# Kernel optimization log

Hardware: AMD Instinct MI355X
Metric: run time of the kernel (lower is better)

The kernel has to match this reference:

```python
import jax, jax.numpy as jnp
import numpy as np
import math

B, S, D, H, HD, FF, L, NS = 16, 512, 256, 8, 32, 1024, 2, 1024
THETA = 10000.0
EPS = 1e-5


def setup_inputs() -> dict:
    key = jax.random.key(0)
    ks = jax.random.split(key, 20)
    n = lambda i, shape: jax.random.normal(ks[i], shape, jnp.float32) * 0.02
    inp = {
        'values': jax.random.normal(ks[0], (B, S), jnp.float32),
        'dib': jax.random.uniform(ks[1], (B, S), jnp.float32),
        'gamma': jax.random.uniform(ks[2], (B, S), jnp.float32),
        'memory_type': jnp.ones((B, S), jnp.float32),
        'key_padding_mask': jnp.ones((B, S), dtype=bool),
        # input projection Linear(5, D)
        'in_w': n(3, (5, D)), 'in_b': jnp.zeros((D,), jnp.float32),
        # per-layer params stacked on leading L axis
        'ln1_s': jnp.ones((L, D), jnp.float32), 'ln1_b': jnp.zeros((L, D), jnp.float32),
        'qw': n(4, (L, D, D)), 'qb': jnp.zeros((L, D), jnp.float32),
        'kw': n(5, (L, D, D)), 'kb': jnp.zeros((L, D), jnp.float32),
        'vw': n(6, (L, D, D)), 'vb': jnp.zeros((L, D), jnp.float32),
        'ow': n(7, (L, D, D)), 'ob': jnp.zeros((L, D), jnp.float32),
        'ln2_s': jnp.ones((L, D), jnp.float32), 'ln2_b': jnp.zeros((L, D), jnp.float32),
        'ffw1': n(8, (L, D, FF)), 'ffb1': jnp.zeros((L, FF), jnp.float32),
        'ffw2': n(9, (L, FF, D)), 'ffb2': jnp.zeros((L, D), jnp.float32),
        'fn_s': jnp.ones((D,), jnp.float32), 'fn_b': jnp.zeros((D,), jnp.float32),
        # output head Linear(S*D, NS)
        'head_w': n(10, (S * D, NS)), 'head_b': jnp.zeros((NS,), jnp.float32),
    }
    return inp


def _layernorm(x, s, b):
    m = jnp.mean(x, axis=-1, keepdims=True)
    v = jnp.mean(jnp.square(x - m), axis=-1, keepdims=True)
    return (x - m) * jax.lax.rsqrt(v + EPS) * s + b


def _rotate_half(x):
    x1, x2 = jnp.split(x, 2, axis=-1)
    return jnp.concatenate((-x2, x1), axis=-1)


def _rope_tables():
    pos = jnp.arange(S, dtype=jnp.float32)
    inv_freq = 1.0 / (THETA ** (jnp.arange(0, HD, 2, dtype=jnp.float32) / HD))
    freqs = pos[:, None] * inv_freq[None, :]           # [S, HD/2]
    emb = jnp.concatenate((freqs, freqs), axis=-1)      # [S, HD]
    return jnp.cos(emb), jnp.sin(emb)


def _forward(values, dib, gamma, memory_type, key_padding_mask,
             in_w, in_b, ln1_s, ln1_b, qw, qb, kw, kb, vw, vb, ow, ob,
             ln2_s, ln2_b, ffw1, ffb1, ffw2, ffb2, fn_s, fn_b, head_w, head_b):
    # token features: (sign, magnitude, gamma, dib, memory_type in {-1,+1})
    sign = jnp.where(values >= 0, 1.0, -1.0)
    mt = memory_type * 2.0 - 1.0  # values in [0,1] -> signed encoding
    features = jnp.stack((sign, jnp.abs(values), gamma, dib, mt), axis=-1)  # [B,S,5]
    x = features @ in_w + in_b  # [B,S,D]

    cos, sin = _rope_tables()  # [S,HD]
    cos4 = cos[None, None]     # [1,1,S,HD]
    sin4 = sin[None, None]
    mask = key_padding_mask    # [B,S] bool
    neg = jnp.finfo(x.dtype).min
    scale = 1.0 / math.sqrt(HD)

    for l in range(L):
        h = _layernorm(x, ln1_s[l], ln1_b[l])
        q = (h @ qw[l] + qb[l]).reshape(B, S, H, HD).transpose(0, 2, 1, 3)  # [B,H,S,HD]
        k = (h @ kw[l] + kb[l]).reshape(B, S, H, HD).transpose(0, 2, 1, 3)
        v = (h @ vw[l] + vb[l]).reshape(B, S, H, HD).transpose(0, 2, 1, 3)
        q = q * cos4 + _rotate_half(q) * sin4
        k = k * cos4 + _rotate_half(k) * sin4
        scores = jnp.einsum('bhqd,bhkd->bhqk', q, k) * scale  # [B,H,S,S]
        scores = jnp.where(mask[:, None, None, :], scores, neg)
        attn = jax.nn.softmax(scores, axis=-1)
        ctx = jnp.einsum('bhqk,bhkd->bhqd', attn, v)
        ctx = ctx.transpose(0, 2, 1, 3).reshape(B, S, D)
        out = (ctx @ ow[l] + ob[l]) * mask[..., None].astype(x.dtype)
        x = x + out
        h2 = _layernorm(x, ln2_s[l], ln2_b[l])
        ff = jax.nn.gelu(h2 @ ffw1[l] + ffb1[l], approximate=False) @ ffw2[l] + ffb2[l]
        x = x + ff

    x = _layernorm(x, fn_s, fn_b)
    logits = x.reshape(B, S * D) @ head_w + head_b  # [B,NS]
    return logits


def reference(values, dib, gamma, memory_type, key_padding_mask,
              in_w, in_b, ln1_s, ln1_b, qw, qb, kw, kb, vw, vb, ow, ob,
              ln2_s, ln2_b, ffw1, ffb1, ffw2, ffb2, fn_s, fn_b, head_w, head_b):
    return _forward(values, dib, gamma, memory_type, key_padding_mask,
                    in_w, in_b, ln1_s, ln1_b, qw, qb, kw, kb, vw, vb, ow, ob,
                    ln2_s, ln2_b, ffw1, ffb1, ffw2, ffb2, fn_s, fn_b, head_w, head_b)
```

## Files before the change

kernel.cpp:

```cpp
#include <hip/hip_runtime.h>
#include <math.h>

#define BB 16
#define SS 512
#define DD 256
#define HH 8
#define HDIM 32
#define FFD 1024
#define NL 2
#define NSOUT 1024
#define SD (SS*DD)
#define ROWS (BB*SS)

#define HEAD_KC 256
#define HEAD_NCH 512

typedef __attribute__((ext_vector_type(8))) short short8;
typedef __attribute__((ext_vector_type(4))) float f32x4;

__device__ __forceinline__ unsigned short f2bf(float f) {
    union { float f; unsigned u; } c; c.f = f;
    unsigned u = c.u + 0x7fffu + ((c.u >> 16) & 1u);
    return (unsigned short)(u >> 16);
}

__global__ __launch_bounds__(256) void k_prep_all(
    const float* __restrict__ p_qw, const float* __restrict__ p_kw,
    const float* __restrict__ p_vw, const float* __restrict__ p_ow,
    const float* __restrict__ p_f1w, const float* __restrict__ p_f2w,
    unsigned short* __restrict__ wq, unsigned short* __restrict__ wk,
    unsigned short* __restrict__ wv, unsigned short* __restrict__ wo,
    unsigned short* __restrict__ wf1, unsigned short* __restrict__ wf2,
    float* __restrict__ ct, float* __restrict__ st) {
    int bid = blockIdx.x;
    int t = threadIdx.x;
    if (bid >= 1536) {
        int i = (bid - 1536) * 256 + t;
        if (i < SS * 16) {
            int s = i >> 4, f = i & 15;
            float invf = powf(10000.f, -(float)f / 16.f);
            float ang = (float)s * invf;
            ct[i] = cosf(ang);
            st[i] = sinf(ang);
        }
        return;
    }
    const float* src; unsigned short* dst;
    int K, N, kx, nx, l;
    if (bid < 512) {
        int grp = bid >> 7, r = bid & 127; l = r >> 6; int tl = r & 63;
        kx = tl >> 3; nx = tl & 7; K = DD; N = DD;
        src = grp == 0 ? p_qw : grp == 1 ? p_kw : grp == 2 ? p_vw : p_ow;
        dst = grp == 0 ? wq : grp == 1 ? wk : grp == 2 ? wv : wo;
    } else if (bid < 1024) {
        int r = bid - 512; l = r >> 8; int tl = r & 255;
        kx = tl >> 5; nx = tl & 31; K = DD; N = FFD; src = p_f1w; dst = wf1;
    } else {
        int r = bid - 1024; l = r >> 8; int tl = r & 255;
        kx = tl >> 3; nx = tl & 7; K = FFD; N = DD; src = p_f2w; dst = wf2;
    }
    __shared__ float tile[32][33];
    size_t zo = (size_t)l * K * N;
    int k0 = kx * 32, n0 = nx * 32;
    int r_ = t >> 3, c4 = (t & 7) * 4;
    float4 a = *(const float4*)&src[zo + (size_t)(k0 + r_) * N + n0 + c4];
    tile[r_][c4 + 0] = a.x; tile[r_][c4 + 1] = a.y; tile[r_][c4 + 2] = a.z; tile[r_][c4 + 3] = a.w;
    __syncthreads();
    unsigned o0 = f2bf(tile[c4 + 0][r_]), o1 = f2bf(tile[c4 + 1][r_]);
    unsigned o2 = f2bf(tile[c4 + 2][r_]), o3 = f2bf(tile[c4 + 3][r_]);
    uint2 ud = { o0 | (o1 << 16), o2 | (o3 << 16) };
    *(uint2*)&dst[zo + (size_t)(n0 + r_) * K + k0 + c4] = ud;
}

__global__ __launch_bounds__(256) void k_input_proj(
    const float* __restrict__ values, const float* __restrict__ dib,
    const float* __restrict__ gamma, const float* __restrict__ mtyp,
    const float* __restrict__ in_w, const float* __restrict__ in_b,
    float* __restrict__ x) {
    int i = blockIdx.x * 256 + threadIdx.x;
    int row = i >> 6, d4 = (i & 63) * 4;
    float v = values[row];
    float f0 = (v >= 0.f) ? 1.f : -1.f;
    float f1 = fabsf(v);
    float f2 = gamma[row];
    float f3 = dib[row];
    float f4 = mtyp[row] * 2.f - 1.f;
    float4 w0 = *(const float4*)&in_w[d4];
    float4 w1 = *(const float4*)&in_w[DD + d4];
    float4 w2 = *(const float4*)&in_w[2 * DD + d4];
    float4 w3 = *(const float4*)&in_w[3 * DD + d4];
    float4 w4 = *(const float4*)&in_w[4 * DD + d4];
    float4 bb = *(const float4*)&in_b[d4];
    float4 o;
    o.x = f0 * w0.x + f1 * w1.x + f2 * w2.x + f3 * w3.x + f4 * w4.x + bb.x;
    o.y = f0 * w0.y + f1 * w1.y + f2 * w2.y + f3 * w3.y + f4 * w4.y + bb.y;
    o.z = f0 * w0.z + f1 * w1.z + f2 * w2.z + f3 * w3.z + f4 * w4.z + bb.z;
    o.w = f0 * w0.w + f1 * w1.w + f2 * w2.w + f3 * w3.w + f4 * w4.w + bb.w;
    *(float4*)&x[(size_t)row * DD + d4] = o;
}

template <bool OBF>
__global__ __launch_bounds__(256) void k_layernorm_w(
    const float* __restrict__ in, void* __restrict__ outp,
    const float* __restrict__ sc, const float* __restrict__ bi) {
    int t = threadIdx.x, lane = t & 63, w = t >> 6;
    int row = blockIdx.x * 4 + w;
    float4 v = *(const float4*)&in[(size_t)row * DD + lane * 4];
    float s1 = v.x + v.y + v.z + v.w;
    float s2 = v.x * v.x + v.y * v.y + v.z * v.z + v.w * v.w;
#pragma unroll
    for (int off = 32; off > 0; off >>= 1) {
        s1 += __shfl_xor(s1, off);
        s2 += __shfl_xor(s2, off);
    }
    float mean = s1 * (1.f / DD);
    float var = s2 * (1.f / DD) - mean * mean;
    float rstd = rsqrtf(var + 1e-5f);
    float4 sv = *(const float4*)&sc[lane * 4];
    float4 bv = *(const float4*)&bi[lane * 4];
    float o0 = (v.x - mean) * rstd * sv.x + bv.x;
    float o1 = (v.y - mean) * rstd * sv.y + bv.y;
    float o2 = (v.z - mean) * rstd * sv.z + bv.z;
    float o3 = (v.w - mean) * rstd * sv.w + bv.w;
    if (OBF) {
        ushort4 u = { f2bf(o0), f2bf(o1), f2bf(o2), f2bf(o3) };
        *(ushort4*)&((unsigned short*)outp)[(size_t)row * DD + lane * 4] = u;
    } else {
        float4 o = { o0, o1, o2, o3 };
        *(float4*)&((float*)outp)[(size_t)row * DD + lane * 4] = o;
    }
}

__global__ __launch_bounds__(256) void k_gemm_ff1(
    const short* __restrict__ A, const short* __restrict__ Bt,
    const float* __restrict__ bias, unsigned short* __restrict__ Cout,
    int M, int N, int K) {
    __shared__ __align__(16) short As[128 * 32];
    __shared__ __align__(16) short Bs[128 * 32];
    int t = threadIdx.x;
    int lane = t & 63, wid = t >> 6;
    int wr = wid >> 1, wc = wid & 1;
    int m0 = blockIdx.x * 128, n0 = blockIdx.y * 128;
    f32x4 acc[4][4] = {};
    int srow = t >> 2, sslot = t & 3;
    for (int k0 = 0; k0 < K; k0 += 32) {
#pragma unroll
        for (int p = 0; p < 2; ++p) {
            int row = srow + p * 64;
            int sw = sslot ^ ((row >> 1) & 3);
            *(float4*)&As[row * 32 + sw * 8] =
                *(const float4*)&A[(size_t)(m0 + row) * K + k0 + sslot * 8];
            *(float4*)&Bs[row * 32 + sw * 8] =
                *(const float4*)&Bt[(size_t)(n0 + row) * K + k0 + sslot * 8];
        }
        __syncthreads();
        short8 af[4], bfr[4];
#pragma unroll
        for (int mt = 0; mt < 4; ++mt) {
            int row = wr * 64 + mt * 16 + (lane & 15);
            int sl = (lane >> 4) ^ ((row >> 1) & 3);
            af[mt] = *(const short8*)&As[row * 32 + sl * 8];
        }
#pragma unroll
        for (int nt = 0; nt < 4; ++nt) {
            int row = wc * 64 + nt * 16 + (lane & 15);
            int sl = (lane >> 4) ^ ((row >> 1) & 3);
            bfr[nt] = *(const short8*)&Bs[row * 32 + sl * 8];
        }
#pragma unroll
        for (int mt = 0; mt < 4; ++mt)
#pragma unroll
            for (int nt = 0; nt < 4; ++nt)
                acc[mt][nt] = __builtin_amdgcn_mfma_f32_16x16x32_bf16(af[mt], bfr[nt], acc[mt][nt], 0, 0, 0);
        __syncthreads();
    }
#pragma unroll
    for (int mt = 0; mt < 4; ++mt) {
#pragma unroll
        for (int i = 0; i < 4; ++i) {
            int gm = m0 + wr * 64 + mt * 16 + (lane >> 4) * 4 + i;
#pragma unroll
            for (int nt = 0; nt < 4; ++nt) {
                int gn = n0 + wc * 64 + nt * 16 + (lane & 15);
                float v = acc[mt][nt][i] + bias[gn];
                v = 0.5f * v * (1.f + erff(v * 0.70710678118654752f));
                Cout[(size_t)gm * N + gn] = f2bf(v);
            }
        }
    }
}

template <int EPI>
__global__ __launch_bounds__(256) void k_gemm64(
    const short* __restrict__ A, const short* __restrict__ Bt,
    const float* __restrict__ bias, float* __restrict__ Cout,
    int M, int N, int K, const float* __restrict__ resx, const int* __restrict__ mask) {
    __shared__ __align__(16) short As[64 * 64];
    __shared__ __align__(16) short Bs[128 * 64];
    int t = threadIdx.x;
    int lane = t & 63, wid = t >> 6;
    int wr = wid >> 1, wc = wid & 1;
    int m0 = blockIdx.x * 64, n0 = blockIdx.y * 128;
    int l15 = lane & 15, lh = lane >> 4;
    f32x4 acc[2][4] = {};
    for (int k0 = 0; k0 < K; k0 += 64) {
#pragma unroll
        for (int p = 0; p < 2; ++p) {
            int idx = t + p * 256;
            int row = idx >> 3, sl = idx & 7;
            int sw = sl ^ (row & 7);
            *(float4*)&As[row * 64 + sw * 8] =
                *(const float4*)&A[(size_t)(m0 + row) * K + k0 + sl * 8];
        }
#pragma unroll
        for (int p = 0; p < 4; ++p) {
            int idx = t + p * 256;
            int row = idx >> 3, sl = idx & 7;
            int sw = sl ^ (row & 7);
            *(float4*)&Bs[row * 64 + sw * 8] =
                *(const float4*)&Bt[(size_t)(n0 + row) * K + k0 + sl * 8];
        }
        __syncthreads();
#pragma unroll
        for (int kk = 0; kk < 2; ++kk) {
            short8 af[2], bfr[4];
#pragma unroll
            for (int mt = 0; mt < 2; ++mt) {
                int row = wr * 32 + mt * 16 + l15;
                int sl = (kk * 4 + lh) ^ (row & 7);
                af[mt] = *(const short8*)&As[row * 64 + sl * 8];
            }
#pragma unroll
            for (int nt = 0; nt < 4; ++nt) {
                int row = wc * 64 + nt * 16 + l15;
                int sl = (kk * 4 + lh) ^ (row & 7);
                bfr[nt] = *(const short8*)&Bs[row * 64 + sl * 8];
            }
#pragma unroll
            for (int mt = 0; mt < 2; ++mt)
#pragma unroll
                for (int nt = 0; nt < 4; ++nt)
                    acc[mt][nt] = __builtin_amdgcn_mfma_f32_16x16x32_bf16(af[mt], bfr[nt], acc[mt][nt], 0, 0, 0);
        }
        __syncthreads();
    }
#pragma unroll
    for (int mt = 0; mt < 2; ++mt) {
#pragma unroll
        for (int i = 0; i < 4; ++i) {
            int gm = m0 + wr * 32 + mt * 16 + lh * 4 + i;
            float mk = 1.f;
            if (EPI == 2) mk = (mask[gm] != 0) ? 1.f : 0.f;
#pragma unroll
            for (int nt = 0; nt < 4; ++nt) {
                int gn = n0 + wc * 64 + nt * 16 + l15;
                float v = acc[mt][nt][i] + bias[gn];
                v = resx[(size_t)gm * N + gn] + v * mk;
                Cout[(size_t)gm * N + gn] = v;
            }
        }
    }
}

__global__ __launch_bounds__(256) void k_qkv64(
    const short* __restrict__ A,
    const short* __restrict__ Wq, const short* __restrict__ Wk, const short* __restrict__ Wv,
    const float* __restrict__ bq, const float* __restrict__ bk, const float* __restrict__ bv,
    const float* __restrict__ ct, const float* __restrict__ st,
    unsigned short* __restrict__ q16, unsigned short* __restrict__ k16,
    unsigned short* __restrict__ vt16) {
    __shared__ __align__(16) short As[64 * 32];
    __shared__ __align__(16) short Bs[128 * 32];
    int mat = blockIdx.y >> 1;
    int n0 = (blockIdx.y & 1) * 128;
    const short* Bt = (mat == 0) ? Wq : (mat == 1) ? Wk : Wv;
    const float* bias = (mat == 0) ? bq : (mat == 1) ? bk : bv;
    int t = threadIdx.x;
    int lane = t & 63, wid = t >> 6;
    int wr = wid >> 1, wc = wid & 1;
    int m0 = blockIdx.x * 64;
    int l15 = lane & 15, lh = lane >> 4;
    f32x4 acc[2][4] = {};
    int srow = t >> 2, sslot = t & 3;
    for (int k0 = 0; k0 < DD; k0 += 32) {
        {
            int sw = sslot ^ ((srow >> 1) & 3);
            *(float4*)&As[srow * 32 + sw * 8] =
                *(const float4*)&A[(size_t)(m0 + srow) * DD + k0 + sslot * 8];
        }
#pragma unroll
        for (int p = 0; p < 2; ++p) {
            int row = srow + p * 64;
            int sw = sslot ^ ((row >> 1) & 3);
            *(float4*)&Bs[row * 32 + sw * 8] =
                *(const float4*)&Bt[(size_t)(n0 + row) * DD + k0 + sslot * 8];
        }
        __syncthreads();
        short8 af[2], bfr[4];
#pragma unroll
        for (int mt = 0; mt < 2; ++mt) {
            int row = wr * 32 + mt * 16 + l15;
            int sl = lh ^ ((row >> 1) & 3);
            af[mt] = *(const short8*)&As[row * 32 + sl * 8];
        }
#pragma unroll
        for (int nt = 0; nt < 4; ++nt) {
            int row = wc * 64 + nt * 16 + l15;
            int sl = lh ^ ((row >> 1) & 3);
            bfr[nt] = *(const short8*)&Bs[row * 32 + sl * 8];
        }
#pragma unroll
        for (int mt = 0; mt < 2; ++mt)
#pragma unroll
            for (int nt = 0; nt < 4; ++nt)
                acc[mt][nt] = __builtin_amdgcn_mfma_f32_16x16x32_bf16(af[mt], bfr[nt], acc[mt][nt], 0, 0, 0);
        __syncthreads();
    }
    float bs[4];
#pragma unroll
    for (int nt = 0; nt < 4; ++nt) bs[nt] = bias[n0 + wc * 64 + nt * 16 + l15];
    if (mat < 2) {
        unsigned short* dst = (mat == 0) ? q16 : k16;
        const float qscale = (mat == 0) ? 0.17677669529663687f : 1.f;
#pragma unroll
        for (int mt = 0; mt < 2; ++mt) {
#pragma unroll
            for (int i = 0; i < 4; ++i) {
                int gm = m0 + wr * 32 + mt * 16 + lh * 4 + i;
                int s = gm & (SS - 1);
                float c = ct[s * 16 + l15], sn = st[s * 16 + l15];
                float val[4];
#pragma unroll
                for (int nt = 0; nt < 4; ++nt) val[nt] = (acc[mt][nt][i] + bs[nt]) * qscale;
#pragma unroll
                for (int nt = 0; nt < 4; ++nt) {
                    float partner = val[nt ^ 1];
                    float o = ((nt & 1) == 0) ? (val[nt] * c - partner * sn)
                                              : (val[nt] * c + partner * sn);
                    dst[(size_t)gm * DD + n0 + wc * 64 + nt * 16 + l15] = f2bf(o);
                }
            }
        }
    } else {
#pragma unroll
        for (int mt = 0; mt < 2; ++mt) {
            int gmb = m0 + wr * 32 + mt * 16 + lh * 4;
            int b = gmb >> 9, sb = gmb & (SS - 1);
#pragma unroll
            for (int nt = 0; nt < 4; ++nt) {
                int gn = n0 + wc * 64 + nt * 16 + l15;
                int h = gn >> 5, d = gn & 31;
                ushort4 u;
#pragma unroll
                for (int i = 0; i < 4; ++i)
                    (&u.x)[i] = f2bf(acc[mt][nt][i] + bs[nt]);
                *(ushort4*)&vt16[((size_t)((b * HH + h) * HDIM + d)) * SS + sb] = u;
            }
        }
    }
}

__global__ __launch_bounds__(256) void k_flash(
    const short* __restrict__ qb, const short* __restrict__ kb,
    const short* __restrict__ vt, const int* __restrict__ mask,
    unsigned short* __restrict__ ctxb) {
    __shared__ float bias_lds[SS];
    __shared__ __align__(16) short p_lds[4][32 * 72];
    __shared__ __align__(16) float r_lds[4][32];
    int t = threadIdx.x, lane = t & 63, wq = t >> 6;
    int bh = blockIdx.y;
    int b = bh >> 3, h = bh & 7;
    int q0 = blockIdx.x * 128 + wq * 32;
    bias_lds[t]       = (mask[b * SS + t]       != 0) ? 0.f : -3.0e38f;
    bias_lds[t + 256] = (mask[b * SS + t + 256] != 0) ? 0.f : -3.0e38f;
    __syncthreads();
    int l15 = lane & 15, lh = lane >> 4;
    short8 qfr[2];
    qfr[0] = *(const short8*)&qb[((size_t)(b * SS) + q0 + l15) * DD + h * HDIM + lh * 8];
    qfr[1] = *(const short8*)&qb[((size_t)(b * SS) + q0 + 16 + l15) * DD + h * HDIM + lh * 8];
    float m[2] = {-3.0e38f, -3.0e38f};
    float lsum[2] = {0.f, 0.f};
    f32x4 oacc[2][2] = {};
    for (int k0 = 0; k0 < SS; k0 += 64) {
        f32x4 sT[4][2];
#pragma unroll
        for (int kt = 0; kt < 4; ++kt) {
            short8 kf = *(const short8*)&kb[((size_t)(b * SS) + k0 + kt * 16 + l15) * DD + h * HDIM + lh * 8];
#pragma unroll
            for (int qf = 0; qf < 2; ++qf) {
                f32x4 z = {0.f, 0.f, 0.f, 0.f};
                sT[kt][qf] = __builtin_amdgcn_mfma_f32_16x16x32_bf16(kf, qfr[qf], z, 0, 0, 0);
            }
        }
        float p[2][16];
        float r[2];
#pragma unroll
        for (int qf = 0; qf < 2; ++qf) {
            float pmax = -3.0e38f;
#pragma unroll
            for (int kt = 0; kt < 4; ++kt)
#pragma unroll
                for (int i = 0; i < 4; ++i) {
                    float s = sT[kt][qf][i] + bias_lds[k0 + kt * 16 + lh * 4 + i];
                    p[qf][kt * 4 + i] = s;
                    pmax = fmaxf(pmax, s);
                }
            pmax = fmaxf(pmax, __shfl_xor(pmax, 16));
            pmax = fmaxf(pmax, __shfl_xor(pmax, 32));
            float mn = fmaxf(m[qf], pmax);
            r[qf] = __expf(m[qf] - mn);
            m[qf] = mn;
            float cs = 0.f;
#pragma unroll
            for (int j = 0; j < 16; ++j) {
                float e = __expf(p[qf][j] - mn);
                p[qf][j] = e;
                cs += e;
            }
            cs += __shfl_xor(cs, 16);
            cs += __shfl_xor(cs, 32);
            lsum[qf] = lsum[qf] * r[qf] + cs;
        }
#pragma unroll
        for (int qf = 0; qf < 2; ++qf) {
            int qq = qf * 16 + l15;
#pragma unroll
            for (int kt = 0; kt < 4; ++kt) {
                unsigned u0 = (unsigned)f2bf(p[qf][kt * 4 + 0]) | ((unsigned)f2bf(p[qf][kt * 4 + 1]) << 16);
                unsigned u1 = (unsigned)f2bf(p[qf][kt * 4 + 2]) | ((unsigned)f2bf(p[qf][kt * 4 + 3]) << 16);
                uint2 u = { u0, u1 };
                *(uint2*)&p_lds[wq][qq * 72 + kt * 16 + lh * 4] = u;
            }
        }
        if (lane < 16) { r_lds[wq][l15] = r[0]; r_lds[wq][16 + l15] = r[1]; }
        __syncthreads();
#pragma unroll
        for (int mf = 0; mf < 2; ++mf) {
            float4 rv = *(const float4*)&r_lds[wq][mf * 16 + lh * 4];
#pragma unroll
            for (int df = 0; df < 2; ++df) {
                oacc[mf][df][0] *= rv.x; oacc[mf][df][1] *= rv.y;
                oacc[mf][df][2] *= rv.z; oacc[mf][df][3] *= rv.w;
            }
        }
#pragma unroll
        for (int ks = 0; ks < 2; ++ks) {
            short8 pa0 = *(const short8*)&p_lds[wq][(l15) * 72 + ks * 32 + lh * 8];
            short8 pa1 = *(const short8*)&p_lds[wq][(16 + l15) * 72 + ks * 32 + lh * 8];
#pragma unroll
            for (int df = 0; df < 2; ++df) {
                short8 vf = *(const short8*)&vt[((size_t)bh * HDIM + df * 16 + l15) * SS + k0 + ks * 32 + lh * 8];
                oacc[0][df] = __builtin_amdgcn_mfma_f32_16x16x32_bf16(pa0, vf, oacc[0][df], 0, 0, 0);
                oacc[1][df] = __builtin_amdgcn_mfma_f32_16x16x32_bf16(pa1, vf, oacc[1][df], 0, 0, 0);
            }
        }
        __syncthreads();
    }
    if (lane < 16) { r_lds[wq][l15] = 1.f / lsum[0]; r_lds[wq][16 + l15] = 1.f / lsum[1]; }
    __syncthreads();
#pragma unroll
    for (int mf = 0; mf < 2; ++mf) {
        float4 lv = *(const float4*)&r_lds[wq][mf * 16 + lh * 4];
        const float li[4] = { lv.x, lv.y, lv.z, lv.w };
#pragma unroll
        for (int df = 0; df < 2; ++df)
#pragma unroll
            for (int i = 0; i < 4; ++i) {
                int gq = q0 + mf * 16 + lh * 4 + i;
                int gd = df * 16 + l15;
                ctxb[((size_t)(b * SS) + gq) * DD + h * HDIM + gd] = f2bf(oacc[mf][df][i] * li[i]);
            }
    }
}

__global__ __launch_bounds__(256) void k_head_part(
    const float* __restrict__ x, const float* __restrict__ fns, const float* __restrict__ fnb,
    const float* __restrict__ W, float* __restrict__ part) {
    __shared__ float xs[16 * HEAD_KC];
    int c = blockIdx.x;
    int t = threadIdx.x, lane = t & 63, w = t >> 6;
    float4 sv = *(const float4*)&fns[lane * 4];
    float4 bv = *(const float4*)&fnb[lane * 4];
#pragma unroll
    for (int rr = 0; rr < 4; ++rr) {
        int b = w * 4 + rr;
        float4 v = *(const float4*)&x[(size_t)b * SD + c * HEAD_KC + lane * 4];
        float s1 = v.x + v.y + v.z + v.w;
        float s2 = v.x * v.x + v.y * v.y + v.z * v.z + v.w * v.w;
#pragma unroll
        for (int off = 32; off > 0; off >>= 1) {
            s1 += __shfl_xor(s1, off);
            s2 += __shfl_xor(s2, off);
        }
        float mean = s1 * (1.f / DD);
        float var = s2 * (1.f / DD) - mean * mean;
        float rstd = rsqrtf(var + 1e-5f);
        float4 o;
        o.x = (v.x - mean) * rstd * sv.x + bv.x;
        o.y = (v.y - mean) * rstd * sv.y + bv.y;
        o.z = (v.z - mean) * rstd * sv.z + bv.z;
        o.w = (v.w - mean) * rstd * sv.w + bv.w;
        *(float4*)&xs[b * HEAD_KC + lane * 4] = o;
    }
    __syncthreads();
    int k0 = c * HEAD_KC;
    int n4 = t * 4;
    float acc[16][4] = {};
#pragma unroll 8
    for (int k = 0; k < HEAD_KC; ++k) {
        f32x4 wv = __builtin_nontemporal_load((const f32x4*)&W[(size_t)(k0 + k) * NSOUT + n4]);
#pragma unroll
        for (int b = 0; b < 16; ++b) {
            float xv = xs[b * HEAD_KC + k];
            acc[b][0] += xv * wv[0]; acc[b][1] += xv * wv[1];
            acc[b][2] += xv * wv[2]; acc[b][3] += xv * wv[3];
        }
    }
#pragma unroll
    for (int b = 0; b < 16; ++b) {
        float4 o = {acc[b][0], acc[b][1], acc[b][2], acc[b][3]};
        *(float4*)&part[((size_t)c * 16 + b) * NSOUT + n4] = o;
    }
}

__global__ __launch_bounds__(512) void k_head_reduce(
    const float* __restrict__ part, const float* __restrict__ hb,
    float* __restrict__ out) {
    __shared__ float red[8][260];
    int t = threadIdx.x;
    int col = t & 63;
    int grp = t >> 6;
    int base = blockIdx.x * 256;
    f32x4 s = {0.f, 0.f, 0.f, 0.f};
#pragma unroll 8
    for (int c = grp; c < HEAD_NCH; c += 8) {
        f32x4 p = *(const f32x4*)&part[(size_t)c * (16 * NSOUT) + base + col * 4];
        s[0] += p[0]; s[1] += p[1]; s[2] += p[2]; s[3] += p[3];
    }
    red[grp][col * 4 + 0] = s[0];
    red[grp][col * 4 + 1] = s[1];
    red[grp][col * 4 + 2] = s[2];
    red[grp][col * 4 + 3] = s[3];
    __syncthreads();
    if (t < 256) {
        float acc = 0.f;
#pragma unroll
        for (int g = 0; g < 8; ++g) acc += red[g][t];
        out[base + t] = acc + hb[(base + t) & (NSOUT - 1)];
    }
}

extern "C" void kernel_launch(void* const* d_in, const int* in_sizes, int n_in,
                              void* d_out, int out_size, void* d_ws, size_t ws_size,
                              hipStream_t stream) {
    const float* values = (const float*)d_in[0];
    const float* dib    = (const float*)d_in[1];
    const float* gamma  = (const float*)d_in[2];
    const float* mtyp   = (const float*)d_in[3];
    const int*   mask   = (const int*)d_in[4];
    const float* in_w   = (const float*)d_in[5];
    const float* in_b   = (const float*)d_in[6];
    const float* ln1_s  = (const float*)d_in[7];
    const float* ln1_b  = (const float*)d_in[8];
    const float* p_qw   = (const float*)d_in[9];
    const float* p_qb   = (const float*)d_in[10];
    const float* p_kw   = (const float*)d_in[11];
    const float* p_kb   = (const float*)d_in[12];
    const float* p_vw   = (const float*)d_in[13];
    const float* p_vb   = (const float*)d_in[14];
    const float* p_ow   = (const float*)d_in[15];
    const float* p_ob   = (const float*)d_in[16];
    const float* ln2_s  = (const float*)d_in[17];
    const float* ln2_b  = (const float*)d_in[18];
    const float* p_f1w  = (const float*)d_in[19];
    const float* p_f1b  = (const float*)d_in[20];
    const float* p_f2w  = (const float*)d_in[21];
    const float* p_f2b  = (const float*)d_in[22];
    const float* fn_s   = (const float*)d_in[23];
    const float* fn_b   = (const float*)d_in[24];
    const float* head_w = (const float*)d_in[25];
    const float* head_b = (const float*)d_in[26];
    float* out = (float*)d_out;

    const size_t MB = 1u << 20;
    char* w = (char*)d_ws;
    float* x    = (float*)(w + 0 * MB);
    unsigned short* h16  = (unsigned short*)(w + 32 * MB);
    unsigned short* q16  = (unsigned short*)(w + 36 * MB);
    unsigned short* k16  = (unsigned short*)(w + 40 * MB);
    unsigned short* vt16 = (unsigned short*)(w + 44 * MB);
    unsigned short* cx16 = (unsigned short*)(w + 48 * MB);
    unsigned short* f116 = (unsigned short*)(w + 52 * MB);
    unsigned short* wq16 = (unsigned short*)(w + 68 * MB);
    unsigned short* wk16 = (unsigned short*)(w + 68 * MB + 256 * 1024);
    unsigned short* wv16 = (unsigned short*)(w + 68 * MB + 512 * 1024);
    unsigned short* wo16 = (unsigned short*)(w + 68 * MB + 768 * 1024);
    unsigned short* wf116 = (unsigned short*)(w + 69 * MB);
    unsigned short* wf216 = (unsigned short*)(w + 70 * MB);
    float* ct   = (float*)(w + 71 * MB);
    float* st   = (float*)(w + 71 * MB + 64 * 1024);
    float* sc   = (float*)(w + 72 * MB);

    k_prep_all<<<1568, 256, 0, stream>>>(p_qw, p_kw, p_vw, p_ow, p_f1w, p_f2w,
                                         wq16, wk16, wv16, wo16, wf116, wf216, ct, st);
    k_input_proj<<<2048, 256, 0, stream>>>(values, dib, gamma, mtyp, in_w, in_b, x);

    for (int l = 0; l < NL; ++l) {
        k_layernorm_w<true><<<2048, 256, 0, stream>>>(x, h16, ln1_s + l * DD, ln1_b + l * DD);
        k_qkv64<<<dim3(128, 6), 256, 0, stream>>>((const short*)h16,
            (const short*)(wq16 + l * 65536), (const short*)(wk16 + l * 65536),
            (const short*)(wv16 + l * 65536),
            p_qb + l * DD, p_kb + l * DD, p_vb + l * DD, ct, st, q16, k16, vt16);
        k_flash<<<dim3(4, BB * HH), 256, 0, stream>>>((const short*)q16, (const short*)k16,
            (const short*)vt16, mask, cx16);
        k_gemm64<2><<<dim3(128, 2), 256, 0, stream>>>((const short*)cx16,
            (const short*)(wo16 + l * 65536), p_ob + l * DD, x, ROWS, DD, DD, x, mask);
        k_layernorm_w<true><<<2048, 256, 0, stream>>>(x, h16, ln2_s + l * DD, ln2_b + l * DD);
        k_gemm_ff1<<<dim3(64, 8), 256, 0, stream>>>((const short*)h16,
            (const short*)(wf116 + l * 262144), p_f1b + l * FFD, f116, ROWS, FFD, DD);
        k_gemm64<3><<<dim3(128, 2), 256, 0, stream>>>((const short*)f116,
            (const short*)(wf216 + l * 262144), p_f2b + l * DD, x, ROWS, DD, FFD, x, nullptr);
    }

    k_head_part<<<HEAD_NCH, 256, 0, stream>>>(x, fn_s, fn_b, head_w, sc);
    k_head_reduce<<<64, 512, 0, stream>>>(sc, head_b, out);
}
```

Before: 344.9 us.

## Fuse layernorm into QKV and FF1 GEMM prologues; use shuffles in flash rescale

Removes the standalone layernorm kernels. The QKV and FF1 GEMMs now load fp32 activations, normalize whole rows into a swizzled LDS tile, and then run the K loop with 64-wide B tiles. This eliminates launches and the bf16 intermediate buffer. In exchange, every column block recomputes the layernorm, and LDS per block grows a lot, which lowers occupancy. The flash kernel replaces LDS-based broadcasting of rescale factors with wave shuffles and drops block-wide barriers.

```diff
diff --git a/kernel.cpp b/kernel.cpp
--- a/kernel.cpp
+++ b/kernel.cpp
@@ -99,13 +99,9 @@
     *(float4*)&x[(size_t)row * DD + d4] = o;
 }
 
-template <bool OBF>
-__global__ __launch_bounds__(256) void k_layernorm_w(
-    const float* __restrict__ in, void* __restrict__ outp,
-    const float* __restrict__ sc, const float* __restrict__ bi) {
-    int t = threadIdx.x, lane = t & 63, w = t >> 6;
-    int row = blockIdx.x * 4 + w;
-    float4 v = *(const float4*)&in[(size_t)row * DD + lane * 4];
+__device__ __forceinline__ float4 ln_row(const float* __restrict__ src, int lane,
+                                         const float4& sv, const float4& bv) {
+    float4 v = *(const float4*)&src[lane * 4];
     float s1 = v.x + v.y + v.z + v.w;
     float s2 = v.x * v.x + v.y * v.y + v.z * v.z + v.w * v.w;
 #pragma unroll
@@ -116,75 +112,81 @@
     float mean = s1 * (1.f / DD);
     float var = s2 * (1.f / DD) - mean * mean;
     float rstd = rsqrtf(var + 1e-5f);
-    float4 sv = *(const float4*)&sc[lane * 4];
-    float4 bv = *(const float4*)&bi[lane * 4];
-    float o0 = (v.x - mean) * rstd * sv.x + bv.x;
-    float o1 = (v.y - mean) * rstd * sv.y + bv.y;
-    float o2 = (v.z - mean) * rstd * sv.z + bv.z;
-    float o3 = (v.w - mean) * rstd * sv.w + bv.w;
-    if (OBF) {
-        ushort4 u = { f2bf(o0), f2bf(o1), f2bf(o2), f2bf(o3) };
-        *(ushort4*)&((unsigned short*)outp)[(size_t)row * DD + lane * 4] = u;
-    } else {
-        float4 o = { o0, o1, o2, o3 };
-        *(float4*)&((float*)outp)[(size_t)row * DD + lane * 4] = o;
-    }
-}
-
-__global__ __launch_bounds__(256) void k_gemm_ff1(
-    const short* __restrict__ A, const short* __restrict__ Bt,
-    const float* __restrict__ bias, unsigned short* __restrict__ Cout,
-    int M, int N, int K) {
-    __shared__ __align__(16) short As[128 * 32];
-    __shared__ __align__(16) short Bs[128 * 32];
+    float4 o;
+    o.x = (v.x - mean) * rstd * sv.x + bv.x;
+    o.y = (v.y - mean) * rstd * sv.y + bv.y;
+    o.z = (v.z - mean) * rstd * sv.z + bv.z;
+    o.w = (v.w - mean) * rstd * sv.w + bv.w;
+    return o;
+}
+
+__global__ __launch_bounds__(256) void k_ff1_fused(
+    const float* __restrict__ x, const float* __restrict__ lns, const float* __restrict__ lnb,
+    const short* __restrict__ Bt, const float* __restrict__ bias,
+    unsigned short* __restrict__ Cout) {
+    __shared__ __align__(16) short Al[128 * 256];
+    __shared__ __align__(16) short Bs[128 * 64];
     int t = threadIdx.x;
     int lane = t & 63, wid = t >> 6;
     int wr = wid >> 1, wc = wid & 1;
     int m0 = blockIdx.x * 128, n0 = blockIdx.y * 128;
+    int l15 = lane & 15, lh = lane >> 4;
+    float4 sv = *(const float4*)&lns[lane * 4];
+    float4 bv = *(const float4*)&lnb[lane * 4];
+    for (int rr = 0; rr < 32; ++rr) {
+        int r = wid * 32 + rr;
+        float4 o = ln_row(&x[(size_t)(m0 + r) * DD], lane, sv, bv);
+        uint2 u = { (unsigned)f2bf(o.x) | ((unsigned)f2bf(o.y) << 16),
+                    (unsigned)f2bf(o.z) | ((unsigned)f2bf(o.w) << 16) };
+        int sl = (lane >> 1) ^ (r & 31);
+        *(uint2*)&Al[r * 256 + sl * 8 + (lane & 1) * 4] = u;
+    }
+    __syncthreads();
     f32x4 acc[4][4] = {};
-    int srow = t >> 2, sslot = t & 3;
-    for (int k0 = 0; k0 < K; k0 += 32) {
-#pragma unroll
-        for (int p = 0; p < 2; ++p) {
-            int row = srow + p * 64;
-            int sw = sslot ^ ((row >> 1) & 3);
-            *(float4*)&As[row * 32 + sw * 8] =
-                *(const float4*)&A[(size_t)(m0 + row) * K + k0 + sslot * 8];
-            *(float4*)&Bs[row * 32 + sw * 8] =
-                *(const float4*)&Bt[(size_t)(n0 + row) * K + k0 + sslot * 8];
+    for (int k0 = 0; k0 < DD; k0 += 64) {
+#pragma unroll
+        for (int p = 0; p < 4; ++p) {
+            int idx = t + p * 256;
+            int row = idx >> 3, sl = idx & 7;
+            int sw = sl ^ (row & 7);
+            *(float4*)&Bs[row * 64 + sw * 8] =
+                *(const float4*)&Bt[(size_t)(n0 + row) * DD + k0 + sl * 8];
         }
         __syncthreads();
-        short8 af[4], bfr[4];
-#pragma unroll
-        for (int mt = 0; mt < 4; ++mt) {
-            int row = wr * 64 + mt * 16 + (lane & 15);
-            int sl = (lane >> 4) ^ ((row >> 1) & 3);
-            af[mt] = *(const short8*)&As[row * 32 + sl * 8];
-        }
-#pragma unroll
-        for (int nt = 0; nt < 4; ++nt) {
-            int row = wc * 64 + nt * 16 + (lane & 15);
-            int sl = (lane >> 4) ^ ((row >> 1) & 3);
-            bfr[nt] = *(const short8*)&Bs[row * 32 + sl * 8];
-        }
-#pragma unroll
-        for (int mt = 0; mt < 4; ++mt)
-#pragma unroll
-            for (int nt = 0; nt < 4; ++nt)
-                acc[mt][nt] = __builtin_amdgcn_mfma_f32_16x16x32_bf16(af[mt], bfr[nt], acc[mt][nt], 0, 0, 0);
+#pragma unroll
+        for (int kk = 0; kk < 2; ++kk) {
+            short8 af[4], bfr[4];
+#pragma unroll
+            for (int mt = 0; mt < 4; ++mt) {
+                int row = wr * 64 + mt * 16 + l15;
+                int sl = ((k0 >> 3) + kk * 4 + lh) ^ (row & 31);
+                af[mt] = *(const short8*)&Al[row * 256 + sl * 8];
+            }
+#pragma unroll
+            for (int nt = 0; nt < 4; ++nt) {
+                int row = wc * 64 + nt * 16 + l15;
+                int sl = (kk * 4 + lh) ^ (row & 7);
+                bfr[nt] = *(const short8*)&Bs[row * 64 + sl * 8];
+            }
+#pragma unroll
+            for (int mt = 0; mt < 4; ++mt)
+#pragma unroll
+                for (int nt = 0; nt < 4; ++nt)
+                    acc[mt][nt] = __builtin_amdgcn_mfma_f32_16x16x32_bf16(af[mt], bfr[nt], acc[mt][nt], 0, 0, 0);
+        }
         __syncthreads();
     }
 #pragma unroll
     for (int mt = 0; mt < 4; ++mt) {
 #pragma unroll
         for (int i = 0; i < 4; ++i) {
-            int gm = m0 + wr * 64 + mt * 16 + (lane >> 4) * 4 + i;
+            int gm = m0 + wr * 64 + mt * 16 + lh * 4 + i;
 #pragma unroll
             for (int nt = 0; nt < 4; ++nt) {
-                int gn = n0 + wc * 64 + nt * 16 + (lane & 15);
+                int gn = n0 + wc * 64 + nt * 16 + l15;
                 float v = acc[mt][nt][i] + bias[gn];
                 v = 0.5f * v * (1.f + erff(v * 0.70710678118654752f));
-                Cout[(size_t)gm * N + gn] = f2bf(v);
+                Cout[(size_t)gm * FFD + gn] = f2bf(v);
             }
         }
     }
@@ -263,14 +265,14 @@
 }
 
 __global__ __launch_bounds__(256) void k_qkv64(
-    const short* __restrict__ A,
+    const float* __restrict__ x, const float* __restrict__ lns, const float* __restrict__ lnb,
     const short* __restrict__ Wq, const short* __restrict__ Wk, const short* __restrict__ Wv,
     const float* __restrict__ bq, const float* __restrict__ bk, const float* __restrict__ bv,
     const float* __restrict__ ct, const float* __restrict__ st,
     unsigned short* __restrict__ q16, unsigned short* __restrict__ k16,
     unsigned short* __restrict__ vt16) {
-    __shared__ __align__(16) short As[64 * 32];
-    __shared__ __align__(16) short Bs[128 * 32];
+    __shared__ __align__(16) short Al[64 * 256];
+    __shared__ __align__(16) short Bs[128 * 64];
     int mat = blockIdx.y >> 1;
     int n0 = (blockIdx.y & 1) * 128;
     const short* Bt = (mat == 0) ? Wq : (mat == 1) ? Wk : Wv;
@@ -280,40 +282,49 @@
     int wr = wid >> 1, wc = wid & 1;
     int m0 = blockIdx.x * 64;
     int l15 = lane & 15, lh = lane >> 4;
+    float4 sv = *(const float4*)&lns[lane * 4];
+    float4 bv4 = *(const float4*)&lnb[lane * 4];
+    for (int rr = 0; rr < 16; ++rr) {
+        int r = wid * 16 + rr;
+        float4 o = ln_row(&x[(size_t)(m0 + r) * DD], lane, sv, bv4);
+        uint2 u = { (unsigned)f2bf(o.x) | ((unsigned)f2bf(o.y) << 16),
+                    (unsigned)f2bf(o.z) | ((unsigned)f2bf(o.w) << 16) };
+        int sl = (lane >> 1) ^ (r & 31);
+        *(uint2*)&Al[r * 256 + sl * 8 + (lane & 1) * 4] = u;
+    }
+    __syncthreads();
     f32x4 acc[2][4] = {};
-    int srow = t >> 2, sslot = t & 3;
-    for (int k0 = 0; k0 < DD; k0 += 32) {
-        {
-            int sw = sslot ^ ((srow >> 1) & 3);
-            *(float4*)&As[srow * 32 + sw * 8] =
-                *(const float4*)&A[(size_t)(m0 + srow) * DD + k0 + sslot * 8];
-        }
-#pragma unroll
-        for (int p = 0; p < 2; ++p) {
-            int row = srow + p * 64;
-            int sw = sslot ^ ((row >> 1) & 3);
-            *(float4*)&Bs[row * 32 + sw * 8] =
-                *(const float4*)&Bt[(size_t)(n0 + row) * DD + k0 + sslot * 8];
+    for (int k0 = 0; k0 < DD; k0 += 64) {
+#pragma unroll
+        for (int p = 0; p < 4; ++p) {
+            int idx = t + p * 256;
+            int row = idx >> 3, sl = idx & 7;
+            int sw = sl ^ (row & 7);
+            *(float4*)&Bs[row * 64 + sw * 8] =
+                *(const float4*)&Bt[(size_t)(n0 + row) * DD + k0 + sl * 8];
         }
         __syncthreads();
-        short8 af[2], bfr[4];
-#pragma unroll
-        for (int mt = 0; mt < 2; ++mt) {
-            int row = wr * 32 + mt * 16 + l15;
-            int sl = lh ^ ((row >> 1) & 3);
-            af[mt] = *(const short8*)&As[row * 32 + sl * 8];
-        }
-#pragma unroll
-        for (int nt = 0; nt < 4; ++nt) {
-            int row = wc * 64 + nt * 16 + l15;
-            int sl = lh ^ ((row >> 1) & 3);
-            bfr[nt] = *(const short8*)&Bs[row * 32 + sl * 8];
-        }
-#pragma unroll
-        for (int mt = 0; mt < 2; ++mt)
-#pragma unroll
-            for (int nt = 0; nt < 4; ++nt)
-                acc[mt][nt] = __builtin_amdgcn_mfma_f32_16x16x32_bf16(af[mt], bfr[nt], acc[mt][nt], 0, 0, 0);
+#pragma unroll
+        for (int kk = 0; kk < 2; ++kk) {
+            short8 af[2], bfr[4];
+#pragma unroll
+            for (int mt = 0; mt < 2; ++mt) {
+                int row = wr * 32 + mt * 16 + l15;
+                int sl = ((k0 >> 3) + kk * 4 + lh) ^ (row & 31);
+                af[mt] = *(const short8*)&Al[row * 256 + sl * 8];
+            }
+#pragma unroll
+            for (int nt = 0; nt < 4; ++nt) {
+                int row = wc * 64 + nt * 16 + l15;
+                int sl = (kk * 4 + lh) ^ (row & 7);
+                bfr[nt] = *(const short8*)&Bs[row * 64 + sl * 8];
+            }
+#pragma unroll
+            for (int mt = 0; mt < 2; ++mt)
+#pragma unroll
+                for (int nt = 0; nt < 4; ++nt)
+                    acc[mt][nt] = __builtin_amdgcn_mfma_f32_16x16x32_bf16(af[mt], bfr[nt], acc[mt][nt], 0, 0, 0);
+        }
         __syncthreads();
     }
     float bs[4];
@@ -366,7 +377,6 @@
     unsigned short* __restrict__ ctxb) {
     __shared__ float bias_lds[SS];
     __shared__ __align__(16) short p_lds[4][32 * 72];
-    __shared__ __align__(16) float r_lds[4][32];
     int t = threadIdx.x, lane = t & 63, wq = t >> 6;
     int bh = blockIdx.y;
     int b = bh >> 3, h = bh & 7;
@@ -432,17 +442,14 @@
                 *(uint2*)&p_lds[wq][qq * 72 + kt * 16 + lh * 4] = u;
             }
         }
-        if (lane < 16) { r_lds[wq][l15] = r[0]; r_lds[wq][16 + l15] = r[1]; }
-        __syncthreads();
-#pragma unroll
-        for (int mf = 0; mf < 2; ++mf) {
-            float4 rv = *(const float4*)&r_lds[wq][mf * 16 + lh * 4];
-#pragma unroll
-            for (int df = 0; df < 2; ++df) {
-                oacc[mf][df][0] *= rv.x; oacc[mf][df][1] *= rv.y;
-                oacc[mf][df][2] *= rv.z; oacc[mf][df][3] *= rv.w;
-            }
-        }
+#pragma unroll
+        for (int mf = 0; mf < 2; ++mf)
+#pragma unroll
+            for (int i = 0; i < 4; ++i) {
+                float rv = __shfl(r[mf], lh * 4 + i);
+                oacc[mf][0][i] *= rv;
+                oacc[mf][1][i] *= rv;
+            }
 #pragma unroll
         for (int ks = 0; ks < 2; ++ks) {
             short8 pa0 = *(const short8*)&p_lds[wq][(l15) * 72 + ks * 32 + lh * 8];
@@ -454,23 +461,19 @@
                 oacc[1][df] = __builtin_amdgcn_mfma_f32_16x16x32_bf16(pa1, vf, oacc[1][df], 0, 0, 0);
             }
         }
-        __syncthreads();
-    }
-    if (lane < 16) { r_lds[wq][l15] = 1.f / lsum[0]; r_lds[wq][16 + l15] = 1.f / lsum[1]; }
-    __syncthreads();
-#pragma unroll
-    for (int mf = 0; mf < 2; ++mf) {
-        float4 lv = *(const float4*)&r_lds[wq][mf * 16 + lh * 4];
-        const float li[4] = { lv.x, lv.y, lv.z, lv.w };
-#pragma unroll
-        for (int df = 0; df < 2; ++df)
-#pragma unroll
-            for (int i = 0; i < 4; ++i) {
-                int gq = q0 + mf * 16 + lh * 4 + i;
+    }
+#pragma unroll
+    for (int mf = 0; mf < 2; ++mf)
+#pragma unroll
+        for (int i = 0; i < 4; ++i) {
+            float li = 1.f / __shfl(lsum[mf], lh * 4 + i);
+            int gq = q0 + mf * 16 + lh * 4 + i;
+#pragma unroll
+            for (int df = 0; df < 2; ++df) {
                 int gd = df * 16 + l15;
-                ctxb[((size_t)(b * SS) + gq) * DD + h * HDIM + gd] = f2bf(oacc[mf][df][i] * li[i]);
-            }
-    }
+                ctxb[((size_t)(b * SS) + gq) * DD + h * HDIM + gd] = f2bf(oacc[mf][df][i] * li);
+            }
+        }
 }
 
 __global__ __launch_bounds__(256) void k_head_part(
@@ -484,22 +487,7 @@
 #pragma unroll
     for (int rr = 0; rr < 4; ++rr) {
         int b = w * 4 + rr;
-        float4 v = *(const float4*)&x[(size_t)b * SD + c * HEAD_KC + lane * 4];
-        float s1 = v.x + v.y + v.z + v.w;
-        float s2 = v.x * v.x + v.y * v.y + v.z * v.z + v.w * v.w;
-#pragma unroll
-        for (int off = 32; off > 0; off >>= 1) {
-            s1 += __shfl_xor(s1, off);
-            s2 += __shfl_xor(s2, off);
-        }
-        float mean = s1 * (1.f / DD);
-        float var = s2 * (1.f / DD) - mean * mean;
-        float rstd = rsqrtf(var + 1e-5f);
-        float4 o;
-        o.x = (v.x - mean) * rstd * sv.x + bv.x;
-        o.y = (v.y - mean) * rstd * sv.y + bv.y;
-        o.z = (v.z - mean) * rstd * sv.z + bv.z;
-        o.w = (v.w - mean) * rstd * sv.w + bv.w;
+        float4 o = ln_row(&x[(size_t)b * SD + c * HEAD_KC], lane, sv, bv);
         *(float4*)&xs[b * HEAD_KC + lane * 4] = o;
     }
     __syncthreads();
@@ -585,7 +573,6 @@
     const size_t MB = 1u << 20;
     char* w = (char*)d_ws;
     float* x    = (float*)(w + 0 * MB);
-    unsigned short* h16  = (unsigned short*)(w + 32 * MB);
     unsigned short* q16  = (unsigned short*)(w + 36 * MB);
     unsigned short* k16  = (unsigned short*)(w + 40 * MB);
     unsigned short* vt16 = (unsigned short*)(w + 44 * MB);
@@ -606,8 +593,7 @@
     k_input_proj<<<2048, 256, 0, stream>>>(values, dib, gamma, mtyp, in_w, in_b, x);
 
     for (int l = 0; l < NL; ++l) {
-        k_layernorm_w<true><<<2048, 256, 0, stream>>>(x, h16, ln1_s + l * DD, ln1_b + l * DD);
-        k_qkv64<<<dim3(128, 6), 256, 0, stream>>>((const short*)h16,
+        k_qkv64<<<dim3(128, 6), 256, 0, stream>>>(x, ln1_s + l * DD, ln1_b + l * DD,
             (const short*)(wq16 + l * 65536), (const short*)(wk16 + l * 65536),
             (const short*)(wv16 + l * 65536),
             p_qb + l * DD, p_kb + l * DD, p_vb + l * DD, ct, st, q16, k16, vt16);
@@ -615,9 +601,8 @@
             (const short*)vt16, mask, cx16);
         k_gemm64<2><<<dim3(128, 2), 256, 0, stream>>>((const short*)cx16,
             (const short*)(wo16 + l * 65536), p_ob + l * DD, x, ROWS, DD, DD, x, mask);
-        k_layernorm_w<true><<<2048, 256, 0, stream>>>(x, h16, ln2_s + l * DD, ln2_b + l * DD);
-        k_gemm_ff1<<<dim3(64, 8), 256, 0, stream>>>((const short*)h16,
-            (const short*)(wf116 + l * 262144), p_f1b + l * FFD, f116, ROWS, FFD, DD);
+        k_ff1_fused<<<dim3(64, 8), 256, 0, stream>>>(x, ln2_s + l * DD, ln2_b + l * DD,
+            (const short*)(wf116 + l * 262144), p_f1b + l * FFD, f116);
         k_gemm64<3><<<dim3(128, 2), 256, 0, stream>>>((const short*)f116,
             (const short*)(wf216 + l * 262144), p_f2b + l * DD, x, ROWS, DD, FFD, x, nullptr);
     }
```

New measurement: 377.6 us. 1.09x slower.
